# Kernel tuning notes

Hardware: AMD Instinct MI355X
Metric: run time of the kernel (lower is better)

The kernel has to match this reference:

```python
import jax, jax.numpy as jnp
import numpy as np

EMBED = 1024
HEADS = 16
HEAD_DIM = EMBED // HEADS


def setup_inputs() -> dict:
    key = jax.random.key(0)
    ks = jax.random.split(key, 12)
    B, S = 2, 2048
    inp = {
        "query": jax.random.normal(ks[0], (B, S, EMBED), dtype=jnp.float32),
        "key": jax.random.normal(ks[1], (B, S, EMBED), dtype=jnp.float32),
        "value": jax.random.normal(ks[2], (B, S, EMBED), dtype=jnp.float32),
        "mask": jnp.ones((B, 1, 1, S), dtype=jnp.int32),
    }
    scale = 1.0 / np.sqrt(EMBED)
    inp["Wq"] = jax.random.normal(ks[3], (EMBED, EMBED), dtype=jnp.float32) * scale
    inp["bq"] = jax.random.normal(ks[4], (EMBED,), dtype=jnp.float32) * 0.01
    inp["Wk"] = jax.random.normal(ks[5], (EMBED, EMBED), dtype=jnp.float32) * scale
    inp["bk"] = jax.random.normal(ks[6], (EMBED,), dtype=jnp.float32) * 0.01
    inp["Wv"] = jax.random.normal(ks[7], (EMBED, EMBED), dtype=jnp.float32) * scale
    inp["bv"] = jax.random.normal(ks[8], (EMBED,), dtype=jnp.float32) * 0.01
    inp["Wo"] = jax.random.normal(ks[9], (EMBED, EMBED), dtype=jnp.float32) * scale
    inp["bo"] = jax.random.normal(ks[10], (EMBED,), dtype=jnp.float32) * 0.01
    return inp


def reference(query, key, value, mask, Wq, bq, Wk, bk, Wv, bv, Wo, bo):
    N, Lq, _ = query.shape
    Lk = key.shape[1]
    # Linear projections (torch Linear: x @ W.T + b)
    q = (query @ Wq.T + bq).reshape(N, Lq, HEADS, HEAD_DIM)
    k = (key @ Wk.T + bk).reshape(N, Lk, HEADS, HEAD_DIM)
    v = (value @ Wv.T + bv).reshape(N, Lk, HEADS, HEAD_DIM)
    # scores: [N, H, Lq, Lk]
    energy = jnp.einsum("nqhd,nkhd->nhqk", q, k)
    energy = jnp.where(mask == 0, jnp.float32(-1e20), energy)
    # NOTE: original scales by sqrt(embedSize), not sqrt(head_dim)
    attn = jax.nn.softmax(energy / jnp.sqrt(jnp.float32(EMBED)), axis=3)
    out = jnp.einsum("nhqv,nvhd->nqhd", attn, v).reshape(N, Lq, EMBED)
    return out @ Wo.T + bo
```

## Files before the change

kernel.cpp:

```cpp
#include <hip/hip_runtime.h>
#include <stdint.h>

typedef unsigned short u16;
typedef __attribute__((ext_vector_type(8))) short short8;
typedef __attribute__((ext_vector_type(4))) short short4v;
typedef __attribute__((ext_vector_type(4))) float floatx4;

#define AS_GLOBAL __attribute__((address_space(1)))
#define AS_LDS    __attribute__((address_space(3)))

#define QSCALE 0.045084220f

__device__ __forceinline__ float bf2f(u16 u) {
  union { unsigned int i; float f; } x; x.i = ((unsigned int)u) << 16; return x.f;
}
__device__ __forceinline__ u16 f2bf(float f) {
  union { float f; unsigned int i; } x; x.f = f;
  unsigned int u = x.i;
  u += 0x7fffu + ((u >> 16) & 1u);
  return (u16)(u >> 16);
}
__device__ __forceinline__ u16 f2bf_fast(float f) {
  union { float f; unsigned int i; } x; x.f = f;
  return (u16)((x.i + 0x8000u) >> 16);
}

__device__ __forceinline__ int probe_is_f32(const void* p) {
  const unsigned int* w = (const unsigned int*)p;
  int cnt = 0;
#pragma unroll
  for (int i = 0; i < 64; ++i) {
    unsigned int lo = w[i] & 0xFFFFu;
    int e = (int)((lo >> 7) & 0xFFu);
    cnt += (e >= 117 && e <= 137) ? 1 : 0;
  }
  return cnt < 32;
}

__device__ __forceinline__ short8 ld8(const void* P, size_t off, int isf32) {
  if (isf32) {
    const float* q = (const float*)P + off;
    float4 x = *(const float4*)q;
    float4 y = *(const float4*)(q + 4);
    short8 r;
    r[0] = (short)f2bf(x.x); r[1] = (short)f2bf(x.y);
    r[2] = (short)f2bf(x.z); r[3] = (short)f2bf(x.w);
    r[4] = (short)f2bf(y.x); r[5] = (short)f2bf(y.y);
    r[6] = (short)f2bf(y.z); r[7] = (short)f2bf(y.w);
    return r;
  }
  return *(const short8*)((const u16*)P + off);
}

__device__ __forceinline__ float ldscalar(const void* P, size_t idx, int isf32) {
  return isf32 ? ((const float*)P)[idx] : bf2f(((const u16*)P)[idx]);
}

__global__ __launch_bounds__(256) void cvt7(
    const void* s0, const void* s1, const void* s2, const void* s3,
    const void* s4, const void* s5, const void* s6,
    u16* d0, u16* d1, u16* d2, u16* d3, u16* d4, u16* d5, u16* d6)
{
  const int z = blockIdx.y;
  const void* src; u16* dst; int n;
  switch (z) {
    case 0: src = s0; dst = d0; n = 4194304; break;
    case 1: src = s1; dst = d1; n = 4194304; break;
    case 2: src = s2; dst = d2; n = 4194304; break;
    case 3: src = s3; dst = d3; n = 1048576; break;
    case 4: src = s4; dst = d4; n = 1048576; break;
    case 5: src = s5; dst = d5; n = 1048576; break;
    default: src = s6; dst = d6; n = 1048576; break;
  }
  const int isf32 = probe_is_f32(src);
  for (int i = blockIdx.x * 256 + threadIdx.x; i * 4 < n; i += gridDim.x * 256) {
    if (isf32) {
      float4 x = ((const float4*)src)[i];
      short4v r;
      r[0] = (short)f2bf(x.x); r[1] = (short)f2bf(x.y);
      r[2] = (short)f2bf(x.z); r[3] = (short)f2bf(x.w);
      *(short4v*)(dst + (size_t)i * 4) = r;
    } else {
      *(short4v*)(dst + (size_t)i * 4) = ((const short4v*)src)[i];
    }
  }
}

__device__ __forceinline__ void gemm_core_bf16(
    const u16* __restrict__ A, const u16* __restrict__ W,
    u16* As, u16* Bs, floatx4 acc[4][4], int m0, int n0, int K, int tid)
{
  const int lane = tid & 63, wv = tid >> 6;
  const int wm = wv >> 1, wn = wv & 1;
  const int g = lane >> 4, ml = lane & 15;
  const int r0 = tid >> 2, kc = (tid & 3) << 3;
  const u16* Ag0 = A + (size_t)(m0 + r0) * K + kc;
  const u16* Ag1 = A + (size_t)(m0 + r0 + 64) * K + kc;
  const u16* Bg0 = W + (size_t)(n0 + r0) * K + kc;
  const u16* Bg1 = W + (size_t)(n0 + r0 + 64) * K + kc;

#define STAGE_QKV(buf_, kt_) do {                                              \
    u16* a0 = As + (buf_) * 4096 + tid * 8;                                    \
    u16* b0 = Bs + (buf_) * 4096 + tid * 8;                                    \
    __builtin_amdgcn_global_load_lds((const AS_GLOBAL unsigned int*)(Ag0 + (kt_)), \
                                     (AS_LDS unsigned int*)a0, 16, 0, 0);      \
    __builtin_amdgcn_global_load_lds((const AS_GLOBAL unsigned int*)(Ag1 + (kt_)), \
                                     (AS_LDS unsigned int*)(a0 + 2048), 16, 0, 0); \
    __builtin_amdgcn_global_load_lds((const AS_GLOBAL unsigned int*)(Bg0 + (kt_)), \
                                     (AS_LDS unsigned int*)b0, 16, 0, 0);      \
    __builtin_amdgcn_global_load_lds((const AS_GLOBAL unsigned int*)(Bg1 + (kt_)), \
                                     (AS_LDS unsigned int*)(b0 + 2048), 16, 0, 0); \
  } while (0)

  STAGE_QKV(0, 0);
  int buf = 0;
#pragma unroll 2
  for (int kt = 0; kt < K; kt += 32) {
    const int nk = (kt + 32 < K) ? (kt + 32) : 0;
    STAGE_QKV(buf ^ 1, nk);
    __asm__ __volatile__("s_waitcnt vmcnt(4)\n\ts_barrier" ::: "memory");
    const u16* Ac = As + buf * 4096;
    const u16* Bc = Bs + buf * 4096;
    short8 af[4], bf[4];
#pragma unroll
    for (int i = 0; i < 4; ++i)
      af[i] = *(const short8*)(Ac + (wm * 64 + i * 16 + ml) * 32 + g * 8);
#pragma unroll
    for (int j = 0; j < 4; ++j)
      bf[j] = *(const short8*)(Bc + (wn * 64 + j * 16 + ml) * 32 + g * 8);
#pragma unroll
    for (int i = 0; i < 4; ++i)
#pragma unroll
      for (int j = 0; j < 4; ++j)
        acc[i][j] = __builtin_amdgcn_mfma_f32_16x16x32_bf16(af[i], bf[j], acc[i][j], 0, 0, 0);
    __asm__ __volatile__("s_waitcnt lgkmcnt(0)\n\ts_barrier" ::: "memory");
    buf ^= 1;
  }
#undef STAGE_QKV
  __asm__ __volatile__("s_waitcnt vmcnt(0)" ::: "memory");
}

__device__ __forceinline__ void gemm_core_cvt(
    const void* __restrict__ A, const void* __restrict__ W, int aF32, int bF32,
    u16* As, u16* Bs, floatx4 acc[4][4], int m0, int n0, int K, int tid)
{
  const int lane = tid & 63, wv = tid >> 6;
  const int wm = wv >> 1, wn = wv & 1;
  const int g = lane >> 4, ml = lane & 15;
  const int r0 = tid >> 2, kc = (tid & 3) << 3;
  const size_t offA0 = (size_t)(m0 + r0) * K + kc;
  const size_t offA1 = (size_t)(m0 + r0 + 64) * K + kc;
  const size_t offB0 = (size_t)(n0 + r0) * K + kc;
  const size_t offB1 = (size_t)(n0 + r0 + 64) * K + kc;
  u16* Al0 = As + tid * 8;  u16* Al1 = As + (tid + 256) * 8;
  u16* Bl0 = Bs + tid * 8;  u16* Bl1 = Bs + (tid + 256) * 8;
  for (int kt = 0; kt < K; kt += 32) {
    short8 a0 = ld8(A, offA0 + kt, aF32);
    short8 a1 = ld8(A, offA1 + kt, aF32);
    short8 b0 = ld8(W, offB0 + kt, bF32);
    short8 b1 = ld8(W, offB1 + kt, bF32);
    *(short8*)Al0 = a0;  *(short8*)Al1 = a1;
    *(short8*)Bl0 = b0;  *(short8*)Bl1 = b1;
    __syncthreads();
    short8 af[4], bf[4];
#pragma unroll
    for (int i = 0; i < 4; ++i)
      af[i] = *(const short8*)(As + (wm * 64 + i * 16 + ml) * 32 + g * 8);
#pragma unroll
    for (int j = 0; j < 4; ++j)
      bf[j] = *(const short8*)(Bs + (wn * 64 + j * 16 + ml) * 32 + g * 8);
#pragma unroll
    for (int i = 0; i < 4; ++i)
#pragma unroll
      for (int j = 0; j < 4; ++j)
        acc[i][j] = __builtin_amdgcn_mfma_f32_16x16x32_bf16(af[i], bf[j], acc[i][j], 0, 0, 0);
    __syncthreads();
  }
}

__device__ __forceinline__ void qkv_epilogue(
    floatx4 acc[4][4], const void* Bi, int cF32, u16* O, int m0, int n0,
    int tid, int z)
{
  const int lane = tid & 63, wv = tid >> 6;
  const int wm = wv >> 1, wn = wv & 1, g = lane >> 4, ml = lane & 15;
  const float sc = (z == 0) ? QSCALE : 1.0f;
#pragma unroll
  for (int j = 0; j < 4; ++j) {
    int gn = n0 + wn * 64 + j * 16 + ml;
    float bvv = ldscalar(Bi, (size_t)gn, cF32);
    int h = gn >> 6, d = gn & 63;
    if (z == 2) {
#pragma unroll
      for (int i = 0; i < 4; ++i) {
        int gm0 = m0 + wm * 64 + i * 16 + g * 4;
        int b = gm0 >> 11, s0 = gm0 & 2047;
        short4v pk;
#pragma unroll
        for (int r = 0; r < 4; ++r) pk[r] = (short)f2bf_fast(acc[i][j][r] + bvv);
        *(short4v*)(O + ((((size_t)b * 16 + h) * 64 + d) * 2048 + s0)) = pk;
      }
    } else {
#pragma unroll
      for (int i = 0; i < 4; ++i)
#pragma unroll
        for (int r = 0; r < 4; ++r) {
          int gm = m0 + wm * 64 + i * 16 + g * 4 + r;
          int b = gm >> 11, s = gm & 2047;
          O[(((size_t)b * 16 + h) * 2048 + s) * 64 + d] =
              f2bf_fast((acc[i][j][r] + bvv) * sc);
        }
    }
  }
}

__global__ __launch_bounds__(256) void qkv_gemm_bf16(
    const u16* __restrict__ Xq, const u16* __restrict__ Xk, const u16* __restrict__ Xv,
    const u16* __restrict__ Wq, const u16* __restrict__ Wk, const u16* __restrict__ Wv,
    const void* __restrict__ Bq, const void* __restrict__ Bk, const void* __restrict__ Bv,
    u16* __restrict__ Oq, u16* __restrict__ Ok, u16* __restrict__ Ov)
{
  __align__(16) __shared__ u16 As[8192];
  __align__(16) __shared__ u16 Bs[8192];
  const int z = blockIdx.z;
  const u16* X = (z == 0) ? Xq : (z == 1) ? Xk : Xv;
  const u16* W = (z == 0) ? Wq : (z == 1) ? Wk : Wv;
  const void* Bi = (z == 0) ? Bq : (z == 1) ? Bk : Bv;
  u16* O = (z == 0) ? Oq : (z == 1) ? Ok : Ov;
  const int tid = threadIdx.x;
  const int m0 = blockIdx.x * 128, n0 = blockIdx.y * 128;
  floatx4 acc[4][4] = {};
  gemm_core_bf16(X, W, As, Bs, acc, m0, n0, 1024, tid);
  const int cF32 = probe_is_f32(Bi);
  qkv_epilogue(acc, Bi, cF32, O, m0, n0, tid, z);
}

__global__ __launch_bounds__(256) void qkv_gemm_cvt(
    const void* __restrict__ Xq, const void* __restrict__ Xk, const void* __restrict__ Xv,
    const void* __restrict__ Wq, const void* __restrict__ Wk, const void* __restrict__ Wv,
    const void* __restrict__ Bq, const void* __restrict__ Bk, const void* __restrict__ Bv,
    u16* __restrict__ Oq, u16* __restrict__ Ok, u16* __restrict__ Ov)
{
  __align__(16) __shared__ u16 As[4096];
  __align__(16) __shared__ u16 Bs[4096];
  const int z = blockIdx.z;
  const void* X  = (z == 0) ? Xq : (z == 1) ? Xk : Xv;
  const void* W  = (z == 0) ? Wq : (z == 1) ? Wk : Wv;
  const void* Bi = (z == 0) ? Bq : (z == 1) ? Bk : Bv;
  u16* O = (z == 0) ? Oq : (z == 1) ? Ok : Ov;
  const int aF32 = probe_is_f32(X);
  const int bF32 = probe_is_f32(W);
  const int cF32 = probe_is_f32(Bi);
  const int tid = threadIdx.x;
  const int m0 = blockIdx.y * 128, n0 = blockIdx.x * 128;
  floatx4 acc[4][4] = {};
  gemm_core_cvt(X, W, aF32, bF32, As, Bs, acc, m0, n0, 1024, tid);
  qkv_epilogue(acc, Bi, cF32, O, m0, n0, tid, z);
}

__global__ __launch_bounds__(256) void out_gemm_bf16(
    const u16* __restrict__ X, const u16* __restrict__ W,
    const void* __restrict__ Bi, float* __restrict__ O)
{
  __align__(16) __shared__ u16 As[8192];
  __align__(16) __shared__ u16 Bs[8192];
  const int tid = threadIdx.x;
  const int m0 = blockIdx.x * 128, n0 = blockIdx.y * 128;
  floatx4 acc[4][4] = {};
  gemm_core_bf16(X, W, As, Bs, acc, m0, n0, 1024, tid);
  const int cF32 = probe_is_f32(Bi);
  const int lane = tid & 63, wv = tid >> 6;
  const int wm = wv >> 1, wn = wv & 1, g = lane >> 4, ml = lane & 15;
#pragma unroll
  for (int j = 0; j < 4; ++j) {
    int gn = n0 + wn * 64 + j * 16 + ml;
    float bvv = ldscalar(Bi, (size_t)gn, cF32);
#pragma unroll
    for (int i = 0; i < 4; ++i)
#pragma unroll
      for (int r = 0; r < 4; ++r) {
        int gm = m0 + wm * 64 + i * 16 + g * 4 + r;
        O[(size_t)gm * 1024 + gn] = acc[i][j][r] + bvv;
      }
  }
}

__global__ __launch_bounds__(256) void out_gemm_cvt(
    const u16* __restrict__ X, const void* __restrict__ W,
    const void* __restrict__ Bi, float* __restrict__ O)
{
  __align__(16) __shared__ u16 As[4096];
  __align__(16) __shared__ u16 Bs[4096];
  const int bF32 = probe_is_f32(W);
  const int cF32 = probe_is_f32(Bi);
  const int tid = threadIdx.x;
  const int m0 = blockIdx.y * 128, n0 = blockIdx.x * 128;
  floatx4 acc[4][4] = {};
  gemm_core_cvt(X, W, 0, bF32, As, Bs, acc, m0, n0, 1024, tid);
  const int lane = tid & 63, wv = tid >> 6;
  const int wm = wv >> 1, wn = wv & 1, g = lane >> 4, ml = lane & 15;
#pragma unroll
  for (int j = 0; j < 4; ++j) {
    int gn = n0 + wn * 64 + j * 16 + ml;
    float bvv = ldscalar(Bi, (size_t)gn, cF32);
#pragma unroll
    for (int i = 0; i < 4; ++i)
#pragma unroll
      for (int r = 0; r < 4; ++r) {
        int gm = m0 + wm * 64 + i * 16 + g * 4 + r;
        O[(size_t)gm * 1024 + gn] = acc[i][j][r] + bvv;
      }
  }
}

__global__ __launch_bounds__(256) void flash_attn(
    const u16* __restrict__ Q, const u16* __restrict__ K, const u16* __restrict__ V,
    const int* __restrict__ Mask, u16* __restrict__ O)
{
  __align__(16) __shared__ u16 Ks[2][64 * 64];
  __align__(16) __shared__ u16 Vt[64 * 64];
  __align__(16) __shared__ u16 Ps[4][16 * 72];
  __align__(16) __shared__ int Ms[64];
  __shared__ int Wok[4];

  const int qt = blockIdx.x;
  const int bh = blockIdx.y;
  const int b = bh >> 4, h = bh & 15;
  const int tid = threadIdx.x;
  const int lane = tid & 63, wv = tid >> 6;
  const int g = lane >> 4, ml = lane & 15;

  const size_t baseQ  = (((size_t)b * 16 + h) * 2048 + (size_t)qt * 64) * 64;
  const size_t baseKV = ((size_t)b * 16 + h) * 2048 * 64;

  {
    int la = 1;
#pragma unroll
    for (int i = 0; i < 8; ++i) la &= Mask[b * 2048 + tid * 8 + i];
    int wall = __all(la != 0);
    if (lane == 0) Wok[wv] = wall;
  }

  short8 qf[2];
#pragma unroll
  for (int ks = 0; ks < 2; ++ks)
    qf[ks] = *(const short8*)(Q + baseQ + (size_t)(wv * 16 + ml) * 64 + ks * 32 + g * 8);

  const u16* kg[2]; const u16* vg[2];
  int lo[2];
#pragma unroll
  for (int t = 0; t < 2; ++t) {
    int s = tid + t * 256;
    int krow = s >> 3, kch = (s & 7) ^ (krow & 7);
    kg[t] = K + baseKV + (size_t)krow * 64 + kch * 8;
    int vd = s >> 3,  vch = (s & 7) ^ (vd & 7);
    vg[t] = V + baseKV + (size_t)vd * 2048 + vch * 8;
    lo[t] = ((tid & 448) + t * 256) * 8;
  }

#pragma unroll
  for (int t = 0; t < 2; ++t)
    __builtin_amdgcn_global_load_lds((const AS_GLOBAL unsigned int*)kg[t],
                                     (AS_LDS unsigned int*)(&Ks[0][0] + lo[t]), 16, 0, 0);

  __syncthreads();
  const bool maskall = Wok[0] && Wok[1] && Wok[2] && Wok[3];

  floatx4 oacc[4] = {};
  float lp[4] = {0.f, 0.f, 0.f, 0.f};

  int buf = 0;
#pragma unroll 2
  for (int kv0 = 0; kv0 < 2048; kv0 += 64) {
#pragma unroll
    for (int t = 0; t < 2; ++t)
      __builtin_amdgcn_global_load_lds((const AS_GLOBAL unsigned int*)(vg[t] + kv0),
                                       (AS_LDS unsigned int*)(Vt + lo[t]), 16, 0, 0);
    const int nxt = (kv0 + 64) & 2047;
#pragma unroll
    for (int t = 0; t < 2; ++t)
      __builtin_amdgcn_global_load_lds((const AS_GLOBAL unsigned int*)(kg[t] + (size_t)nxt * 64),
                                       (AS_LDS unsigned int*)(&Ks[buf ^ 1][0] + lo[t]), 16, 0, 0);
    if (!maskall && tid < 64) Ms[tid] = Mask[b * 2048 + kv0 + tid];
    __asm__ __volatile__("s_waitcnt vmcnt(4) lgkmcnt(0)\n\ts_barrier" ::: "memory");

    const u16* Kc = &Ks[buf][0];
    float sv[4][4];
    __builtin_amdgcn_s_setprio(1);
#pragma unroll
    for (int j = 0; j < 4; ++j) {
      floatx4 a = {0.f, 0.f, 0.f, 0.f};
      int row = j * 16 + ml;
#pragma unroll
      for (int ks = 0; ks < 2; ++ks) {
        short8 kb = *(const short8*)(Kc + row * 64 + ((((ks << 2) + g) ^ (row & 7)) << 3));
        a = __builtin_amdgcn_mfma_f32_16x16x32_bf16(qf[ks], kb, a, 0, 0, 0);
      }
#pragma unroll
      for (int r = 0; r < 4; ++r) sv[j][r] = a[r];
    }
    __builtin_amdgcn_s_setprio(0);
    if (!maskall) {
      int mok[4];
#pragma unroll
      for (int j = 0; j < 4; ++j) mok[j] = Ms[j * 16 + ml];
#pragma unroll
      for (int j = 0; j < 4; ++j)
#pragma unroll
        for (int r = 0; r < 4; ++r)
          sv[j][r] = (mok[j] == 0) ? -1.0e30f : sv[j][r];
    }

#pragma unroll
    for (int j = 0; j < 4; ++j)
#pragma unroll
      for (int r = 0; r < 4; ++r) {
        float p = __builtin_amdgcn_exp2f(sv[j][r]);
        sv[j][r] = p;
        lp[r] += p;
      }

#pragma unroll
    for (int j = 0; j < 4; ++j)
#pragma unroll
      for (int r = 0; r < 4; ++r)
        Ps[wv][(g * 4 + r) * 72 + j * 16 + ml] = f2bf_fast(sv[j][r]);

    __asm__ __volatile__("s_waitcnt vmcnt(2)\n\ts_barrier" ::: "memory");
    __asm__ __volatile__("s_waitcnt lgkmcnt(0)" ::: "memory");

    short8 pa[2];
#pragma unroll
    for (int j2 = 0; j2 < 2; ++j2)
      pa[j2] = *(const short8*)(&Ps[wv][ml * 72 + j2 * 32 + g * 8]);
    __builtin_amdgcn_s_setprio(1);
#pragma unroll
    for (int t = 0; t < 4; ++t)
#pragma unroll
      for (int j2 = 0; j2 < 2; ++j2) {
        short8 vb = *(const short8*)(Vt + (t * 16 + ml) * 64 + ((((j2 << 2) + g) ^ (ml & 7)) << 3));
        oacc[t] = __builtin_amdgcn_mfma_f32_16x16x32_bf16(pa[j2], vb, oacc[t], 0, 0, 0);
      }
    __builtin_amdgcn_s_setprio(0);

    __asm__ __volatile__("s_barrier" ::: "memory");
    buf ^= 1;
  }
  __asm__ __volatile__("s_waitcnt vmcnt(0)" ::: "memory");

  float inv[4];
#pragma unroll
  for (int r = 0; r < 4; ++r) {
    float l = lp[r];
    l += __shfl_xor(l, 1);
    l += __shfl_xor(l, 2);
    l += __shfl_xor(l, 4);
    l += __shfl_xor(l, 8);
    inv[r] = (l > 0.f) ? 1.0f / l : 0.f;
  }
#pragma unroll
  for (int t = 0; t < 4; ++t)
#pragma unroll
    for (int r = 0; r < 4; ++r) {
      int q = qt * 64 + wv * 16 + g * 4 + r;
      int d = t * 16 + ml;
      O[((size_t)b * 2048 + q) * 1024 + h * 64 + d] = f2bf_fast(oacc[t][r] * inv[r]);
    }
}

extern "C" void kernel_launch(void* const* d_in, const int* in_sizes, int n_in,
                              void* d_out, int out_size, void* d_ws, size_t ws_size,
                              hipStream_t stream) {
  const void* q_in = d_in[0];
  const void* k_in = d_in[1];
  const void* v_in = d_in[2];
  const int* mask = (const int*)d_in[3];
  const void* Wq = d_in[4];  const void* bq = d_in[5];
  const void* Wk = d_in[6];  const void* bk = d_in[7];
  const void* Wv = d_in[8];  const void* bv = d_in[9];
  const void* Wo = d_in[10]; const void* bo = d_in[11];

  const size_t NTOK = (size_t)2 * 2048 * 1024;
  const size_t NW   = (size_t)1024 * 1024;

  if (ws_size >= (size_t)67108864) {
    u16* CXq = (u16*)d_ws;
    u16* CXk = CXq + NTOK;
    u16* CXv = CXk + NTOK;
    u16* CWq = CXv + NTOK;
    u16* CWk = CWq + NW;
    u16* CWv = CWk + NW;
    u16* CWo = CWv + NW;
    u16* Qp  = CWo + NW;
    u16* Kp  = Qp + NTOK;
    u16* Vp  = Kp + NTOK;
    u16* Ao  = Vp + NTOK;

    cvt7<<<dim3(1024, 7), 256, 0, stream>>>(q_in, k_in, v_in, Wq, Wk, Wv, Wo,
                                            CXq, CXk, CXv, CWq, CWk, CWv, CWo);
    qkv_gemm_bf16<<<dim3(32, 8, 3), 256, 0, stream>>>(CXq, CXk, CXv,
                                                      CWq, CWk, CWv,
                                                      bq, bk, bv, Qp, Kp, Vp);
    flash_attn<<<dim3(32, 32), 256, 0, stream>>>(Qp, Kp, Vp, mask, Ao);
    out_gemm_bf16<<<dim3(32, 8), 256, 0, stream>>>(Ao, CWo, bo, (float*)d_out);
  } else {
    u16* Qp = (u16*)d_ws;
    u16* Kp = Qp + NTOK;
    u16* Vp = Kp + NTOK;
    u16* Ao = Vp + NTOK;

    qkv_gemm_cvt<<<dim3(8, 32, 3), 256, 0, stream>>>(q_in, k_in, v_in,
                                                     Wq, Wk, Wv, bq, bk, bv,
                                                     Qp, Kp, Vp);
    flash_attn<<<dim3(32, 32), 256, 0, stream>>>(Qp, Kp, Vp, mask, Ao);
    out_gemm_cvt<<<dim3(8, 32), 256, 0, stream>>>(Ao, Wo, bo, (float*)d_out);
  }
}
```

Before: 266.0 us.

## Keep P in registers via transposed QK^T MFMA and permlane swaps

The QK^T MFMA swaps its operands so each lane holds a column of scores. The P probabilities are then packed to bf16 with v_cvt_pk_bf16_f32 and rearranged into the PV A-operand layout with permlane32/16 swaps. This removes the per-wave LDS round-trip for P, along with its store, lgkmcnt wait and reload. The row-sum is now accumulated per lane and redistributed with shuffles at the end, and mask lookups change to match the transposed layout. The register-permutation correctness depends on the exact MFMA lane layout on this hardware.

```diff
diff --git a/kernel.cpp b/kernel.cpp
--- a/kernel.cpp
+++ b/kernel.cpp
@@ -5,6 +5,8 @@
 typedef __attribute__((ext_vector_type(8))) short short8;
 typedef __attribute__((ext_vector_type(4))) short short4v;
 typedef __attribute__((ext_vector_type(4))) float floatx4;
+typedef __attribute__((ext_vector_type(2))) unsigned int uint2v;
+typedef __attribute__((ext_vector_type(4))) unsigned int uint4v;
 
 #define AS_GLOBAL __attribute__((address_space(1)))
 #define AS_LDS    __attribute__((address_space(3)))
@@ -23,6 +25,29 @@
 __device__ __forceinline__ u16 f2bf_fast(float f) {
   union { float f; unsigned int i; } x; x.f = f;
   return (u16)((x.i + 0x8000u) >> 16);
+}
+
+__device__ __forceinline__ unsigned int cvtpk_bf16(float lo, float hi) {
+  unsigned int w;
+  __asm__("v_cvt_pk_bf16_f32 %0, %1, %2" : "=v"(w) : "v"(lo), "v"(hi));
+  return w;
+}
+
+__device__ __forceinline__ void pl32_swap(unsigned int& a, unsigned int& b) {
+#if __has_builtin(__builtin_amdgcn_permlane32_swap)
+  uint2v r = __builtin_amdgcn_permlane32_swap(a, b, false, false);
+  a = r[0]; b = r[1];
+#else
+  __asm__("v_permlane32_swap_b32 %0, %1" : "+v"(a), "+v"(b));
+#endif
+}
+__device__ __forceinline__ void pl16_swap(unsigned int& a, unsigned int& b) {
+#if __has_builtin(__builtin_amdgcn_permlane16_swap)
+  uint2v r = __builtin_amdgcn_permlane16_swap(a, b, false, false);
+  a = r[0]; b = r[1];
+#else
+  __asm__("v_permlane16_swap_b32 %0, %1" : "+v"(a), "+v"(b));
+#endif
 }
 
 __device__ __forceinline__ int probe_is_f32(const void* p) {
@@ -319,7 +344,6 @@
 {
   __align__(16) __shared__ u16 Ks[2][64 * 64];
   __align__(16) __shared__ u16 Vt[64 * 64];
-  __align__(16) __shared__ u16 Ps[4][16 * 72];
   __align__(16) __shared__ int Ms[64];
   __shared__ int Wok[4];
 
@@ -367,7 +391,7 @@
   const bool maskall = Wok[0] && Wok[1] && Wok[2] && Wok[3];
 
   floatx4 oacc[4] = {};
-  float lp[4] = {0.f, 0.f, 0.f, 0.f};
+  float lp = 0.f;
 
   int buf = 0;
 #pragma unroll 2
@@ -394,21 +418,18 @@
 #pragma unroll
       for (int ks = 0; ks < 2; ++ks) {
         short8 kb = *(const short8*)(Kc + row * 64 + ((((ks << 2) + g) ^ (row & 7)) << 3));
-        a = __builtin_amdgcn_mfma_f32_16x16x32_bf16(qf[ks], kb, a, 0, 0, 0);
+        a = __builtin_amdgcn_mfma_f32_16x16x32_bf16(kb, qf[ks], a, 0, 0, 0);
       }
 #pragma unroll
       for (int r = 0; r < 4; ++r) sv[j][r] = a[r];
     }
     __builtin_amdgcn_s_setprio(0);
     if (!maskall) {
-      int mok[4];
-#pragma unroll
-      for (int j = 0; j < 4; ++j) mok[j] = Ms[j * 16 + ml];
 #pragma unroll
       for (int j = 0; j < 4; ++j)
 #pragma unroll
         for (int r = 0; r < 4; ++r)
-          sv[j][r] = (mok[j] == 0) ? -1.0e30f : sv[j][r];
+          if (Ms[j * 16 + g * 4 + r] == 0) sv[j][r] = -1.0e30f;
     }
 
 #pragma unroll
@@ -417,22 +438,40 @@
       for (int r = 0; r < 4; ++r) {
         float p = __builtin_amdgcn_exp2f(sv[j][r]);
         sv[j][r] = p;
-        lp[r] += p;
-      }
-
+        lp += p;
+      }
+
+    unsigned int Wd[4][2];
 #pragma unroll
     for (int j = 0; j < 4; ++j)
 #pragma unroll
-      for (int r = 0; r < 4; ++r)
-        Ps[wv][(g * 4 + r) * 72 + j * 16 + ml] = f2bf_fast(sv[j][r]);
+      for (int w = 0; w < 2; ++w)
+        Wd[j][w] = cvtpk_bf16(sv[j][2 * w], sv[j][2 * w + 1]);
+
+    unsigned int Zl[2][2], Zh[2][2];
+#pragma unroll
+    for (int jd = 0; jd < 2; ++jd)
+#pragma unroll
+      for (int w = 0; w < 2; ++w) {
+        unsigned int ua = Wd[2 * jd][w];
+        unsigned int ub = Wd[2 * jd + 1][w];
+        pl32_swap(ua, ub);
+        pl16_swap(ua, ub);
+        Zl[jd][w] = ua;
+        Zh[jd][w] = ub;
+      }
+
+    short8 pa[2];
+#pragma unroll
+    for (int ks = 0; ks < 2; ++ks) {
+      uint4v pw;
+      pw[0] = Zl[ks][0]; pw[1] = Zl[ks][1];
+      pw[2] = Zh[ks][0]; pw[3] = Zh[ks][1];
+      pa[ks] = __builtin_bit_cast(short8, pw);
+    }
 
     __asm__ __volatile__("s_waitcnt vmcnt(2)\n\ts_barrier" ::: "memory");
-    __asm__ __volatile__("s_waitcnt lgkmcnt(0)" ::: "memory");
-
-    short8 pa[2];
-#pragma unroll
-    for (int j2 = 0; j2 < 2; ++j2)
-      pa[j2] = *(const short8*)(&Ps[wv][ml * 72 + j2 * 32 + g * 8]);
+
     __builtin_amdgcn_s_setprio(1);
 #pragma unroll
     for (int t = 0; t < 4; ++t)
@@ -448,15 +487,14 @@
   }
   __asm__ __volatile__("s_waitcnt vmcnt(0)" ::: "memory");
 
+  float l = lp;
+  l += __shfl_xor(l, 16);
+  l += __shfl_xor(l, 32);
   float inv[4];
 #pragma unroll
   for (int r = 0; r < 4; ++r) {
-    float l = lp[r];
-    l += __shfl_xor(l, 1);
-    l += __shfl_xor(l, 2);
-    l += __shfl_xor(l, 4);
-    l += __shfl_xor(l, 8);
-    inv[r] = (l > 0.f) ? 1.0f / l : 0.f;
+    float lr = __shfl(l, (lane & 48) | (((lane >> 4) & 3) * 4 + r));
+    inv[r] = (lr > 0.f) ? 1.0f / lr : 0.f;
   }
 #pragma unroll
   for (int t = 0; t < 4; ++t)
```

New measurement: 250.0 us. 1.06x faster.
